# Kernel optimization log

Hardware: AMD Instinct MI355X
Metric: run time of the kernel (lower is better)

The kernel has to match this reference:

```python
import jax, jax.numpy as jnp
import numpy as np

B, I, H, S = 16384, 256, 256, 32
EVENT_THRESH = 0.85


def setup_inputs() -> dict:
    key = jax.random.key(0)
    ks = jax.random.split(key, 20)
    r = lambda k, shp: jax.random.normal(k, shp, dtype=jnp.float32)
    w = lambda k, shp: jax.random.normal(k, shp, dtype=jnp.float32) * 0.02
    return {
        # forward args / state
        "x_t": r(ks[0], (B, I)),
        "h_lstm": r(ks[1], (B, H)),
        "c_lstm": r(ks[2], (B, H)),
        "h_mem_prev": jnp.zeros((B, H), jnp.float32),
        "slots": r(ks[3], (B, S, I)),
        "ptr": jax.random.randint(ks[4], (B,), 0, S, dtype=jnp.int64),
        # SequenceMemoryCell params (weights stored as (in, out))
        "W_val": w(ks[5], (I, I)),
        "b_val": jnp.zeros((I,), jnp.float32),
        "W_ev": w(ks[6], (I, 1)),
        "b_ev": jnp.zeros((1,), jnp.float32),
        "pos_emb": r(ks[7], (S, I)),
        "slot_weights": jnp.ones((S,), jnp.float32),
        "W_sp": w(ks[8], (I, H)),
        "b_sp": jnp.zeros((H,), jnp.float32),
        # LSTM params
        "W_ih": w(ks[9], (I + H, 4 * H)),
        "b_ih": jnp.zeros((4 * H,), jnp.float32),
        "W_hh": w(ks[10], (H, 4 * H)),
    }


def reference(x_t, h_lstm, c_lstm, h_mem_prev, slots, ptr,
              W_val, b_val, W_ev, b_ev, pos_emb, slot_weights, W_sp, b_sp,
              W_ih, b_ih, W_hh):
    n_slots = slot_weights.shape[0]
    # --- SequenceMemoryCell ---
    e_t = jax.nn.sigmoid(x_t @ W_ev + b_ev)            # (B, 1)
    v = x_t @ W_val + b_val                            # (B, I)
    event_mask = e_t[:, 0] > EVENT_THRESH              # (B,)
    # circular-buffer scatter write at ptr, gated by event_mask
    onehot = jnp.arange(n_slots)[None, :] == ptr[:, None]          # (B, S)
    write = event_mask[:, None] & onehot                           # (B, S)
    new_slots = jnp.where(write[:, :, None], v[:, None, :], slots) # (B, S, I)
    new_ptr = (ptr + event_mask.astype(ptr.dtype)) % n_slots
    # weighted pool over slots with positional embeddings
    w = jax.nn.softmax(slot_weights)                               # (S,)
    pooled = jnp.einsum('bsi,s->bi', new_slots + pos_emb[None], w) # (B, I)
    h_mem = pooled @ W_sp + b_sp                                   # (B, H)
    # --- LSTM on [x_t; h_mem] ---
    gates = jnp.concatenate([x_t, h_mem], axis=1) @ W_ih + b_ih + h_lstm @ W_hh
    i_g, f_g, g_t, o_g = jnp.split(gates, 4, axis=1)
    c_new = jax.nn.sigmoid(f_g) * c_lstm + jax.nn.sigmoid(i_g) * jnp.tanh(g_t)
    h_new = jax.nn.sigmoid(o_g) * jnp.tanh(c_new)
    return (h_new, c_new, h_mem, new_slots, new_ptr)
```

## Files before the change

kernel.cpp:

```cpp
#include <hip/hip_runtime.h>
#include <hip/hip_bf16.h>

#define B_SZ 16384
#define I_SZ 256
#define H_SZ 256
#define S_SZ 32

typedef __attribute__((ext_vector_type(8))) short short8;
typedef __attribute__((ext_vector_type(4))) float f32x4;

__device__ __forceinline__ ushort f2b(float f) {
  __hip_bfloat16 h = __float2bfloat16(f);
  return *reinterpret_cast<ushort*>(&h);
}
__device__ __forceinline__ float sgm(float x) { return 1.0f / (1.0f + expf(-x)); }

__device__ __forceinline__ void gll16(const void* g, void* l) {
  __builtin_amdgcn_global_load_lds(
      (const __attribute__((address_space(1))) unsigned*)g,
      (__attribute__((address_space(3))) unsigned*)l, 16, 0, 0);
}

__global__ __launch_bounds__(256) void prep_weights(
    const float* __restrict__ W_sp, const float* __restrict__ W_ih,
    const float* __restrict__ W_hh, ushort* __restrict__ WspT,
    ushort* __restrict__ WcatT) {
  int idx = blockIdx.x * 256 + threadIdx.x;
  if (idx < 256 * 256) {
    int n = idx >> 8, k = idx & 255;
    WspT[idx] = f2b(W_sp[k * 256 + n]);
  } else {
    int j = idx - 256 * 256;
    int r = j / 768, k = j - r * 768;
    int hb = r >> 6, g = (r >> 4) & 3, hl = r & 15;
    int n = g * 256 + hb * 16 + hl;
    float v = (k < 512) ? W_ih[k * 1024 + n] : W_hh[(k - 512) * 1024 + n];
    WcatT[j] = f2b(v);
  }
}

__global__ __launch_bounds__(256) void event_pool(
    const float* __restrict__ x_t, const float* __restrict__ h_lstm,
    const float* __restrict__ slots, const int* __restrict__ ptr,
    const float* __restrict__ W_val, const float* __restrict__ b_val,
    const float* __restrict__ W_ev, const float* __restrict__ b_ev,
    const float* __restrict__ pos_emb, const float* __restrict__ slot_w,
    float* __restrict__ out_slots, float* __restrict__ out_ptr,
    ushort* __restrict__ x_b, ushort* __restrict__ hl_b,
    ushort* __restrict__ pooled_b) {
  int l = threadIdx.x & 63;
  int w = threadIdx.x >> 6;
  int b = blockIdx.x * 4 + w;
  __shared__ float x_sh[4][256];

  float4 x4 = *(const float4*)(x_t + (size_t)b * 256 + l * 4);
  *(float4*)&x_sh[w][l * 4] = x4;
  ushort4 xb = make_ushort4(f2b(x4.x), f2b(x4.y), f2b(x4.z), f2b(x4.w));
  *(ushort4*)&x_b[(size_t)b * 256 + l * 4] = xb;
  float4 hl4 = *(const float4*)(h_lstm + (size_t)b * 256 + l * 4);
  ushort4 hb = make_ushort4(f2b(hl4.x), f2b(hl4.y), f2b(hl4.z), f2b(hl4.w));
  *(ushort4*)&hl_b[(size_t)b * 256 + l * 4] = hb;

  float4 we4 = *(const float4*)(W_ev + l * 4);
  float p = x4.x * we4.x + x4.y * we4.y + x4.z * we4.z + x4.w * we4.w;
  for (int off = 32; off; off >>= 1) p += __shfl_xor(p, off, 64);
  float z = p + b_ev[0];
  bool ev = sgm(z) > 0.85f;
  int pb = ptr[b];

  __syncthreads();

  float4 v4 = make_float4(0.f, 0.f, 0.f, 0.f);
  if (ev) {
    v4 = *(const float4*)(b_val + l * 4);
    for (int k = 0; k < 256; k++) {
      float xv = x_sh[w][k];
      float4 wv = *(const float4*)(W_val + (size_t)k * 256 + l * 4);
      v4.x += xv * wv.x; v4.y += xv * wv.y;
      v4.z += xv * wv.z; v4.w += xv * wv.w;
    }
  }

  float mx = -1e30f;
  for (int s = 0; s < 32; s++) mx = fmaxf(mx, slot_w[s]);
  float sum = 0.f;
  for (int s = 0; s < 32; s++) sum += expf(slot_w[s] - mx);
  float rs = 1.f / sum;

  const float4* sl4 = (const float4*)slots + (size_t)b * 2048;
  float4* os4 = (float4*)out_slots + (size_t)b * 2048;
  const float4* pe4 = (const float4*)pos_emb;
  float4 pool = make_float4(0.f, 0.f, 0.f, 0.f);
#pragma unroll 8
  for (int s = 0; s < 32; s++) {
    float ws_ = expf(slot_w[s] - mx) * rs;
    float4 t = sl4[s * 64 + l];
    if (ev && s == pb) t = v4;
    os4[s * 64 + l] = t;
    float4 pe = pe4[s * 64 + l];
    pool.x += ws_ * (t.x + pe.x);
    pool.y += ws_ * (t.y + pe.y);
    pool.z += ws_ * (t.z + pe.z);
    pool.w += ws_ * (t.w + pe.w);
  }
  ushort4 pb4 = make_ushort4(f2b(pool.x), f2b(pool.y), f2b(pool.z), f2b(pool.w));
  *(ushort4*)&pooled_b[(size_t)b * 256 + l * 4] = pb4;

  if (l == 0) out_ptr[b] = (float)(ev ? ((pb + 1) & 31) : pb);
}

template <int KTOT, int NTOT, int EPI>
__global__ __launch_bounds__(256) void gemm_bf16(
    const ushort* __restrict__ A0, const ushort* __restrict__ A1,
    const ushort* __restrict__ A2, const ushort* __restrict__ WT,
    const float* __restrict__ bias, float* __restrict__ out_f32,
    ushort* __restrict__ out_b16, const float* __restrict__ c_lstm,
    float* __restrict__ h_out, float* __restrict__ c_out) {
  int l = threadIdx.x & 63;
  int wid = threadIdx.x >> 6;
  int wm = wid >> 1, wn = wid & 1;
  int m0 = blockIdx.x * 128;
  int n0 = blockIdx.y * 128;
  __shared__ ushort Ash[128 * 32];
  __shared__ ushort Bsh[128 * 32];

  f32x4 acc[4][4] = {};

  for (int k0 = 0; k0 < KTOT; k0 += 32) {
    const ushort* As = (k0 < 256) ? A0 : ((k0 < 512) ? A1 : A2);
    int kc = k0 & 255;
#pragma unroll
    for (int i = 0; i < 2; i++) {
      int seg = i * 256 + threadIdx.x;
      int row = seg >> 2, cb = (seg & 3) * 8;
      gll16(As + (size_t)(m0 + row) * 256 + kc + cb, Ash + seg * 8);
    }
#pragma unroll
    for (int i = 0; i < 2; i++) {
      int seg = i * 256 + threadIdx.x;
      int row = seg >> 2, cb = (seg & 3) * 8;
      gll16(WT + (size_t)(n0 + row) * KTOT + k0 + cb, Bsh + seg * 8);
    }
    __syncthreads();

    short8 af[4], bfr[4];
#pragma unroll
    for (int m = 0; m < 4; m++)
      af[m] = *(const short8*)&Ash[(wm * 64 + m * 16 + (l & 15)) * 32 + (l >> 4) * 8];
#pragma unroll
    for (int n = 0; n < 4; n++)
      bfr[n] = *(const short8*)&Bsh[(wn * 64 + n * 16 + (l & 15)) * 32 + (l >> 4) * 8];
#pragma unroll
    for (int m = 0; m < 4; m++)
#pragma unroll
      for (int n = 0; n < 4; n++)
        acc[m][n] = __builtin_amdgcn_mfma_f32_16x16x32_bf16(af[m], bfr[n], acc[m][n], 0, 0, 0);
    __syncthreads();
  }

  if constexpr (EPI == 0) {
#pragma unroll
    for (int m = 0; m < 4; m++)
#pragma unroll
      for (int n = 0; n < 4; n++)
#pragma unroll
        for (int r = 0; r < 4; r++) {
          int row = m0 + wm * 64 + m * 16 + (l >> 4) * 4 + r;
          int col = n0 + wn * 64 + n * 16 + (l & 15);
          float v = acc[m][n][r] + bias[col];
          out_f32[(size_t)row * NTOT + col] = v;
          out_b16[(size_t)row * NTOT + col] = f2b(v);
        }
  } else {
    int h = ((n0 >> 6) + wn) * 16 + (l & 15);
    float bi = bias[h], bf_ = bias[256 + h], bg = bias[512 + h], bo = bias[768 + h];
#pragma unroll
    for (int m = 0; m < 4; m++)
#pragma unroll
      for (int r = 0; r < 4; r++) {
        int row = m0 + wm * 64 + m * 16 + (l >> 4) * 4 + r;
        float ig = acc[m][0][r] + bi;
        float fg = acc[m][1][r] + bf_;
        float gt = acc[m][2][r] + bg;
        float og = acc[m][3][r] + bo;
        float c = c_lstm[(size_t)row * 256 + h];
        float cn = sgm(fg) * c + sgm(ig) * tanhf(gt);
        float hn = sgm(og) * tanhf(cn);
        c_out[(size_t)row * 256 + h] = cn;
        h_out[(size_t)row * 256 + h] = hn;
      }
  }
}

extern "C" void kernel_launch(void* const* d_in, const int* in_sizes, int n_in,
                              void* d_out, int out_size, void* d_ws, size_t ws_size,
                              hipStream_t stream) {
  const float* x_t    = (const float*)d_in[0];
  const float* h_lstm = (const float*)d_in[1];
  const float* c_lstm = (const float*)d_in[2];
  const float* slots  = (const float*)d_in[4];
  const int*   ptr    = (const int*)d_in[5];
  const float* W_val  = (const float*)d_in[6];
  const float* b_val  = (const float*)d_in[7];
  const float* W_ev   = (const float*)d_in[8];
  const float* b_ev   = (const float*)d_in[9];
  const float* pos_emb = (const float*)d_in[10];
  const float* slot_w  = (const float*)d_in[11];
  const float* W_sp   = (const float*)d_in[12];
  const float* b_sp   = (const float*)d_in[13];
  const float* W_ih   = (const float*)d_in[14];
  const float* b_ih   = (const float*)d_in[15];
  const float* W_hh   = (const float*)d_in[16];

  float* out = (float*)d_out;
  const size_t BH = (size_t)B_SZ * H_SZ;
  float* out_h    = out;
  float* out_c    = out + BH;
  float* out_hmem = out + 2 * BH;
  float* out_slots = out + 3 * BH;
  float* out_ptr   = out + 3 * BH + (size_t)B_SZ * S_SZ * I_SZ;

  char* ws = (char*)d_ws;
  ushort* x_b      = (ushort*)(ws);
  ushort* hl_b     = (ushort*)(ws + 8388608);
  ushort* pooled_b = (ushort*)(ws + 16777216);
  ushort* hmem_b   = (ushort*)(ws + 25165824);
  ushort* WspT     = (ushort*)(ws + 33554432);
  ushort* WcatT    = (ushort*)(ws + 33685504);

  prep_weights<<<3328, 256, 0, stream>>>(W_sp, W_ih, W_hh, WspT, WcatT);

  event_pool<<<B_SZ / 4, 256, 0, stream>>>(
      x_t, h_lstm, slots, ptr, W_val, b_val, W_ev, b_ev, pos_emb, slot_w,
      out_slots, out_ptr, x_b, hl_b, pooled_b);

  gemm_bf16<256, 256, 0><<<dim3(128, 2), 256, 0, stream>>>(
      pooled_b, pooled_b, pooled_b, WspT, b_sp, out_hmem, hmem_b,
      nullptr, nullptr, nullptr);

  gemm_bf16<768, 1024, 2><<<dim3(128, 8), 256, 0, stream>>>(
      x_b, hmem_b, hl_b, WcatT, b_ih, nullptr, nullptr,
      c_lstm, out_h, out_c);
}
```

Before: 304.9 us.

## Rewrite LSTM gate GEMM as 256x256 tile double-buffered pipelined kernel

Replaces the generic 128x128 LSTM gate GEMM with a dedicated 512-thread kernel using 256x256 output tiles and 64-wide K steps. The new kernel double-buffers LDS with XOR-swizzled layouts, issues async global-to-LDS loads interleaved with MFMA phases under manual vmcnt waits and raised priority, and remaps block IDs so tiles are grouped per XCD. The intent is to increase operand reuse, hide memory latency and avoid LDS bank conflicts. In exchange it uses more LDS and registers per block and launches only 256 blocks, which lowers occupancy and makes the hand-written wait counts fragile.

```diff
diff --git a/kernel.cpp b/kernel.cpp
--- a/kernel.cpp
+++ b/kernel.cpp
@@ -109,13 +109,10 @@
   if (l == 0) out_ptr[b] = (float)(ev ? ((pb + 1) & 31) : pb);
 }
 
-template <int KTOT, int NTOT, int EPI>
-__global__ __launch_bounds__(256) void gemm_bf16(
-    const ushort* __restrict__ A0, const ushort* __restrict__ A1,
-    const ushort* __restrict__ A2, const ushort* __restrict__ WT,
+__global__ __launch_bounds__(256) void gemm_hmem(
+    const ushort* __restrict__ A0, const ushort* __restrict__ WT,
     const float* __restrict__ bias, float* __restrict__ out_f32,
-    ushort* __restrict__ out_b16, const float* __restrict__ c_lstm,
-    float* __restrict__ h_out, float* __restrict__ c_out) {
+    ushort* __restrict__ out_b16) {
   int l = threadIdx.x & 63;
   int wid = threadIdx.x >> 6;
   int wm = wid >> 1, wn = wid & 1;
@@ -126,20 +123,18 @@
 
   f32x4 acc[4][4] = {};
 
-  for (int k0 = 0; k0 < KTOT; k0 += 32) {
-    const ushort* As = (k0 < 256) ? A0 : ((k0 < 512) ? A1 : A2);
-    int kc = k0 & 255;
+  for (int k0 = 0; k0 < 256; k0 += 32) {
 #pragma unroll
     for (int i = 0; i < 2; i++) {
       int seg = i * 256 + threadIdx.x;
       int row = seg >> 2, cb = (seg & 3) * 8;
-      gll16(As + (size_t)(m0 + row) * 256 + kc + cb, Ash + seg * 8);
+      gll16(A0 + (size_t)(m0 + row) * 256 + k0 + cb, Ash + seg * 8);
     }
 #pragma unroll
     for (int i = 0; i < 2; i++) {
       int seg = i * 256 + threadIdx.x;
       int row = seg >> 2, cb = (seg & 3) * 8;
-      gll16(WT + (size_t)(n0 + row) * KTOT + k0 + cb, Bsh + seg * 8);
+      gll16(WT + (size_t)(n0 + row) * 256 + k0 + cb, Bsh + seg * 8);
     }
     __syncthreads();
 
@@ -158,38 +153,156 @@
     __syncthreads();
   }
 
-  if constexpr (EPI == 0) {
-#pragma unroll
-    for (int m = 0; m < 4; m++)
-#pragma unroll
-      for (int n = 0; n < 4; n++)
-#pragma unroll
-        for (int r = 0; r < 4; r++) {
-          int row = m0 + wm * 64 + m * 16 + (l >> 4) * 4 + r;
-          int col = n0 + wn * 64 + n * 16 + (l & 15);
-          float v = acc[m][n][r] + bias[col];
-          out_f32[(size_t)row * NTOT + col] = v;
-          out_b16[(size_t)row * NTOT + col] = f2b(v);
-        }
-  } else {
-    int h = ((n0 >> 6) + wn) * 16 + (l & 15);
-    float bi = bias[h], bf_ = bias[256 + h], bg = bias[512 + h], bo = bias[768 + h];
-#pragma unroll
-    for (int m = 0; m < 4; m++)
+#pragma unroll
+  for (int m = 0; m < 4; m++)
+#pragma unroll
+    for (int n = 0; n < 4; n++)
 #pragma unroll
       for (int r = 0; r < 4; r++) {
         int row = m0 + wm * 64 + m * 16 + (l >> 4) * 4 + r;
-        float ig = acc[m][0][r] + bi;
-        float fg = acc[m][1][r] + bf_;
-        float gt = acc[m][2][r] + bg;
-        float og = acc[m][3][r] + bo;
-        float c = c_lstm[(size_t)row * 256 + h];
-        float cn = sgm(fg) * c + sgm(ig) * tanhf(gt);
-        float hn = sgm(og) * tanhf(cn);
-        c_out[(size_t)row * 256 + h] = cn;
-        h_out[(size_t)row * 256 + h] = hn;
+        int col = n0 + wn * 64 + n * 16 + (l & 15);
+        float v = acc[m][n][r] + bias[col];
+        out_f32[(size_t)row * 256 + col] = v;
+        out_b16[(size_t)row * 256 + col] = f2b(v);
       }
-  }
+}
+
+template <int KTOT>
+__global__ __launch_bounds__(512) void gemm256_lstm(
+    const ushort* __restrict__ A0s, const ushort* __restrict__ A1s,
+    const ushort* __restrict__ A2s, const ushort* __restrict__ WT,
+    const float* __restrict__ bias, const float* __restrict__ c_lstm,
+    float* __restrict__ h_out, float* __restrict__ c_out) {
+  constexpr int NT = KTOT / 64;
+  __shared__ ushort Ash[2][2][128][64];
+  __shared__ ushort Bsh[2][2][128][64];
+  const int tid = threadIdx.x;
+  const int l = tid & 63;
+  const int wid = tid >> 6;
+  const int wm = wid >> 2, wn = wid & 3;
+  const int id = blockIdx.x;
+  const int xcd = id & 7, jj = id >> 3;
+  const int mb = xcd * 8 + (jj >> 2), nb = jj & 3;
+  const int m0 = mb * 256, n0 = nb * 256;
+
+  auto asel = [&](int kt) { return kt < 4 ? A0s : (kt < 8 ? A1s : A2s); };
+
+  auto stageA = [&](int bu, int h, int kt) {
+    const ushort* s = asel(kt);
+    int cb = (kt & 3) * 64;
+#pragma unroll
+    for (int ld = 0; ld < 2; ld++) {
+      int seg = ld * 512 + tid;
+      int row = seg >> 3, C = seg & 7;
+      int Cs = C ^ (row & 7);
+      gll16(s + (size_t)(m0 + h * 128 + row) * 256 + cb + Cs * 8,
+            &Ash[bu][h][0][0] + seg * 8);
+    }
+  };
+  auto stageB = [&](int bu, int h, int kt) {
+    int cb = kt * 64;
+#pragma unroll
+    for (int ld = 0; ld < 2; ld++) {
+      int seg = ld * 512 + tid;
+      int row = seg >> 3, C = seg & 7;
+      int Cs = C ^ (row & 7);
+      gll16(WT + (size_t)(n0 + h * 128 + row) * KTOT + cb + Cs * 8,
+            &Bsh[bu][h][0][0] + seg * 8);
+    }
+  };
+
+  f32x4 acc[8][4] = {};
+
+  stageB(0, 0, 0); stageB(0, 1, 0);
+  stageA(0, 0, 0); stageA(0, 1, 0);
+  stageB(1, 0, 1); stageB(1, 1, 1);
+
+  for (int t = 0; t < NT; t++) {
+    const int c = t & 1;
+    const ushort* Abase = &Ash[c][wm][0][0];
+    const ushort* Bbase = &Bsh[c][wn >> 1][0][0];
+
+    if (t < NT - 1) asm volatile("s_waitcnt vmcnt(4)" ::: "memory");
+    else            asm volatile("s_waitcnt vmcnt(0)" ::: "memory");
+    asm volatile("s_barrier" ::: "memory");
+
+    short8 bfr[4][2];
+#pragma unroll
+    for (int nf = 0; nf < 4; nf++)
+#pragma unroll
+      for (int kk = 0; kk < 2; kk++) {
+        int r = (wn & 1) * 64 + nf * 16 + (l & 15);
+        int C = (kk * 4 + (l >> 4)) ^ (l & 7);
+        bfr[nf][kk] = *(const short8*)(Bbase + r * 64 + C * 8);
+      }
+    short8 af[2][2];
+#pragma unroll
+    for (int q = 0; q < 2; q++)
+#pragma unroll
+      for (int kk = 0; kk < 2; kk++) {
+        int r = (0 * 2 + q) * 16 + (l & 15);
+        int C = (kk * 4 + (l >> 4)) ^ (l & 7);
+        af[q][kk] = *(const short8*)(Abase + r * 64 + C * 8);
+      }
+    if (t + 1 < NT) stageA(c ^ 1, 0, t + 1);
+    __builtin_amdgcn_s_setprio(1);
+#pragma unroll
+    for (int q = 0; q < 2; q++)
+#pragma unroll
+      for (int nf = 0; nf < 4; nf++)
+#pragma unroll
+        for (int kk = 0; kk < 2; kk++)
+          acc[q][nf] = __builtin_amdgcn_mfma_f32_16x16x32_bf16(
+              af[q][kk], bfr[nf][kk], acc[q][nf], 0, 0, 0);
+    __builtin_amdgcn_s_setprio(0);
+
+#pragma unroll
+    for (int p = 1; p < 4; p++) {
+      asm volatile("s_barrier" ::: "memory");
+#pragma unroll
+      for (int q = 0; q < 2; q++)
+#pragma unroll
+        for (int kk = 0; kk < 2; kk++) {
+          int r = (p * 2 + q) * 16 + (l & 15);
+          int C = (kk * 4 + (l >> 4)) ^ (l & 7);
+          af[q][kk] = *(const short8*)(Abase + r * 64 + C * 8);
+        }
+      if (p == 1) {
+        if (t + 1 < NT) stageA(c ^ 1, 1, t + 1);
+        if (t + 2 < NT) stageB(c, 0, t + 2);
+      } else if (p == 2) {
+        if (t + 2 < NT) stageB(c, 1, t + 2);
+      }
+      __builtin_amdgcn_s_setprio(1);
+#pragma unroll
+      for (int q = 0; q < 2; q++)
+#pragma unroll
+        for (int nf = 0; nf < 4; nf++)
+#pragma unroll
+          for (int kk = 0; kk < 2; kk++)
+            acc[p * 2 + q][nf] = __builtin_amdgcn_mfma_f32_16x16x32_bf16(
+                af[q][kk], bfr[nf][kk], acc[p * 2 + q][nf], 0, 0, 0);
+      __builtin_amdgcn_s_setprio(0);
+    }
+  }
+
+  int h = (nb * 4 + wn) * 16 + (l & 15);
+  float bi = bias[h], bf_ = bias[256 + h], bg = bias[512 + h], bo = bias[768 + h];
+#pragma unroll
+  for (int mf = 0; mf < 8; mf++)
+#pragma unroll
+    for (int r = 0; r < 4; r++) {
+      int row = m0 + wm * 128 + mf * 16 + (l >> 4) * 4 + r;
+      float ig = acc[mf][0][r] + bi;
+      float fg = acc[mf][1][r] + bf_;
+      float gt = acc[mf][2][r] + bg;
+      float og = acc[mf][3][r] + bo;
+      float cc = c_lstm[(size_t)row * 256 + h];
+      float cn = sgm(fg) * cc + sgm(ig) * tanhf(gt);
+      float hn = sgm(og) * tanhf(cn);
+      c_out[(size_t)row * 256 + h] = cn;
+      h_out[(size_t)row * 256 + h] = hn;
+    }
 }
 
 extern "C" void kernel_launch(void* const* d_in, const int* in_sizes, int n_in,
@@ -234,11 +347,9 @@
       x_t, h_lstm, slots, ptr, W_val, b_val, W_ev, b_ev, pos_emb, slot_w,
       out_slots, out_ptr, x_b, hl_b, pooled_b);
 
-  gemm_bf16<256, 256, 0><<<dim3(128, 2), 256, 0, stream>>>(
-      pooled_b, pooled_b, pooled_b, WspT, b_sp, out_hmem, hmem_b,
-      nullptr, nullptr, nullptr);
-
-  gemm_bf16<768, 1024, 2><<<dim3(128, 8), 256, 0, stream>>>(
-      x_b, hmem_b, hl_b, WcatT, b_ih, nullptr, nullptr,
-      c_lstm, out_h, out_c);
-}
+  gemm_hmem<<<dim3(128, 2), 256, 0, stream>>>(
+      pooled_b, WspT, b_sp, out_hmem, hmem_b);
+
+  gemm256_lstm<768><<<256, 512, 0, stream>>>(
+      x_b, hmem_b, hl_b, WcatT, b_ih, c_lstm, out_h, out_c);
+}
```

New measurement: 288.4 us. -5.4%, faster.
